# Kernel tuning notes

Hardware: AMD Instinct MI355X
Metric: run time of the kernel (lower is better)

Reference implementation:

```python
import jax, jax.numpy as jnp
import numpy as np

B, L, NW, H, HID, E, NL, DL = 32, 1024, 512, 768, 384, 4, 12, 128


def setup_inputs() -> dict:
    key = jax.random.key(0)
    ks = jax.random.split(key, 16)
    f = lambda k, s: jax.random.normal(k, s, dtype=jnp.float32) * 0.02
    z = lambda s: jnp.zeros(s, jnp.float32)
    return {
        "token_embs": jax.random.normal(ks[0], (B, L, H), dtype=jnp.float32),
        "word_maps": jnp.sort(jax.random.randint(ks[1], (B, L), 0, NW), axis=-1),
        "lang_ids": jax.random.randint(ks[2], (B,), 0, NL),
        # BiLSTM params (PyTorch gate order i,f,g,o packed along dim 0)
        "Wih_f": f(ks[3], (4 * HID, H)), "Whh_f": f(ks[4], (4 * HID, HID)),
        "bih_f": z((4 * HID,)), "bhh_f": z((4 * HID,)),
        "Wih_b": f(ks[5], (4 * HID, H)), "Whh_b": f(ks[6], (4 * HID, HID)),
        "bih_b": z((4 * HID,)), "bhh_b": z((4 * HID,)),
        "proj_W": f(ks[7], (H, 2 * HID)), "proj_b": z((H,)),
        "lang_table": f(ks[8], (NL, DL)),
        "gate_W1": f(ks[9], (H, H + DL)), "gate_b1": z((H,)),
        "gate_W2": f(ks[10], (E, H)), "gate_b2": z((E,)),
        # stacked expert heads: row i is expert i's (H,1) linear
        "ef_W": f(ks[11], (E, H)), "ef_b": z((E,)),
        "ed_W": f(ks[12], (E, H)), "ed_b": z((E,)),
    }


def _seg_mean(embs, wmap):
    # embs: [L, H], wmap: [L] -> [NW, H] per-word mean of subword embeddings
    sums = jax.ops.segment_sum(embs, wmap, num_segments=NW)
    cnt = jax.ops.segment_sum(jnp.ones(embs.shape[:1], embs.dtype), wmap, num_segments=NW)
    return sums / jnp.maximum(cnt, 1.0)[:, None]


def _lstm(x, Wih, Whh, bih, bhh, reverse):
    # x: [B, T, H] -> hidden states [B, T, HID]; gate order i,f,g,o
    def step(carry, xg):
        h, c = carry
        g = xg + h @ Whh.T + bhh
        i, fg, gg, o = jnp.split(g, 4, axis=-1)
        c = jax.nn.sigmoid(fg) * c + jax.nn.sigmoid(i) * jnp.tanh(gg)
        h = jax.nn.sigmoid(o) * jnp.tanh(c)
        return (h, c), h
    xg = jnp.swapaxes(x @ Wih.T + bih, 0, 1)  # [T, B, 4*HID], input proj hoisted
    init = (jnp.zeros((x.shape[0], Whh.shape[1]), x.dtype),) * 2
    _, hs = jax.lax.scan(step, init, xg, reverse=reverse)
    return jnp.swapaxes(hs, 0, 1)


def reference(token_embs, word_maps, lang_ids, Wih_f, Whh_f, bih_f, bhh_f,
              Wih_b, Whh_b, bih_b, bhh_b, proj_W, proj_b, lang_table,
              gate_W1, gate_b1, gate_W2, gate_b2, ef_W, ef_b, ed_W, ed_b):
    # subword -> word segment-mean pooling, batched
    word_embs = jax.vmap(_seg_mean)(token_embs, word_maps)          # [B, NW, H]
    hf = _lstm(word_embs, Wih_f, Whh_f, bih_f, bhh_f, False)        # [B, NW, HID]
    hb = _lstm(word_embs, Wih_b, Whh_b, bih_b, bhh_b, True)         # [B, NW, HID]
    seq = jnp.concatenate([hf, hb], axis=-1) @ proj_W.T + proj_b    # [B, NW, H]
    # dropout omitted (eval mode)
    gate_in = jnp.concatenate([token_embs[:, 0], lang_table[lang_ids]], axis=-1)  # [B, H+DL]
    gate = jax.nn.softmax(
        jax.nn.relu(gate_in @ gate_W1.T + gate_b1) @ gate_W2.T + gate_b2, axis=-1)  # [B, E]
    fix = jnp.einsum('bwe,be->bw', seq @ ef_W.T + ef_b, gate)       # [B, NW]
    dur = jnp.einsum('bwe,be->bw', seq @ ed_W.T + ed_b, gate)       # [B, NW]
    return (fix, dur)
```

## Files before the change

### kernel.cpp

```cpp
#include <hip/hip_runtime.h>
#include <stdint.h>

#define BB 32
#define LL 1024
#define NW 512
#define HH 768
#define HID 384
#define G4 1536
#define EE 4
#define DLL 128
#define GIN 896
#define CWG 12
#define WGC 32
#define HPAD 392

typedef __attribute__((ext_vector_type(8))) short short8;
typedef __attribute__((ext_vector_type(4))) float f32x4;
typedef __attribute__((ext_vector_type(4))) unsigned int u32x4;
typedef __attribute__((ext_vector_type(2))) unsigned int u32x2;

__device__ __forceinline__ float bf2f(short s){
  union { unsigned int u; float f; } v; v.u = ((unsigned int)(unsigned short)s) << 16; return v.f;
}
__device__ __forceinline__ short f2bf(float f){
  union { float f; unsigned int u; } v; v.f = f;
  unsigned int r = v.u + 0x7fffu + ((v.u >> 16) & 1u);
  return (short)(r >> 16);
}
__device__ __forceinline__ float sigm(float x){ return 1.f / (1.f + __expf(-x)); }
__device__ __forceinline__ float ftanh(float x){ float e = __expf(2.f * x); return 1.f - 2.f / (e + 1.f); }

__device__ __forceinline__ void gload16(const void* g, void* l){
  __builtin_amdgcn_global_load_lds(
      (const __attribute__((address_space(1))) unsigned int*)g,
      (__attribute__((address_space(3))) unsigned int*)l, 16, 0, 0);
}

__global__ void k_f2bf(const float* in, short* out, int n){
  int i = blockIdx.x * blockDim.x + threadIdx.x;
  int st = gridDim.x * blockDim.x;
  for (; i < n; i += st) out[i] = f2bf(in[i]);
}

__global__ __launch_bounds__(256) void k_segmean(const float* __restrict__ tok,
                                                 const int* __restrict__ wmap,
                                                 short* __restrict__ we_bf){
  int blk = blockIdx.x;
  int b = blk >> 9;
  int w = blk & 511;
  const int* m = wmap + b * LL;
  int lo = 0, hi = LL;
  while (lo < hi){ int mid = (lo + hi) >> 1; if (m[mid] < w) lo = mid + 1; else hi = mid; }
  int s = lo;
  int lo2 = s, hi2 = LL;
  while (lo2 < hi2){ int mid = (lo2 + hi2) >> 1; if (m[mid] <= w) lo2 = mid + 1; else hi2 = mid; }
  int e = lo2;
  float cnt = (float)(e - s);
  float denom = fmaxf(cnt, 1.f);
  for (int j = threadIdx.x; j < HH; j += 256){
    float acc = 0.f;
    for (int r = s; r < e; ++r) acc += tok[((size_t)b * LL + r) * HH + j];
    we_bf[((size_t)b * NW + w) * HH + j] = f2bf(acc / denom);
  }
}

__global__ __launch_bounds__(256) void k_gemm_bt(const short* __restrict__ Abf,
                                                 const short* __restrict__ Wbf,
                                                 const float* __restrict__ b1,
                                                 const float* __restrict__ b2,
                                                 float* __restrict__ Cf,
                                                 int M, int N, int K){
  __shared__ __attribute__((aligned(16))) short As[128 * 32];
  __shared__ __attribute__((aligned(16))) short Bs[128 * 32];
  int ntiles = N >> 7;
  int m0 = (blockIdx.x / ntiles) << 7;
  int n0 = (blockIdx.x % ntiles) << 7;
  int tid = threadIdx.x, lane = tid & 63, wv = tid >> 6;
  int wm = (wv >> 1) << 6, wn = (wv & 1) << 6;
  f32x4 acc[4][4] = {};
  for (int kk = 0; kk < K; kk += 32){
#pragma unroll
    for (int q = 0; q < 2; ++q){
      int e = q * 256 + tid;
      int row = e >> 2, col = (e & 3) << 3;
      gload16(Abf + (size_t)(m0 + row) * K + kk + col, As + e * 8);
      gload16(Wbf + (size_t)(n0 + row) * K + kk + col, Bs + e * 8);
    }
    __syncthreads();
    short8 af[4], bfr[4];
#pragma unroll
    for (int x = 0; x < 4; ++x){
      af[x]  = *(const short8*)(As + (wm + x * 16 + (lane & 15)) * 32 + ((lane >> 4) << 3));
      bfr[x] = *(const short8*)(Bs + (wn + x * 16 + (lane & 15)) * 32 + ((lane >> 4) << 3));
    }
#pragma unroll
    for (int x = 0; x < 4; ++x)
#pragma unroll
      for (int y = 0; y < 4; ++y)
        acc[x][y] = __builtin_amdgcn_mfma_f32_16x16x32_bf16(af[x], bfr[y], acc[x][y], 0, 0, 0);
    __syncthreads();
  }
#pragma unroll
  for (int x = 0; x < 4; ++x)
#pragma unroll
    for (int y = 0; y < 4; ++y)
#pragma unroll
      for (int i = 0; i < 4; ++i){
        int mm = m0 + wm + x * 16 + ((lane >> 4) << 2) + i;
        int nn = n0 + wn + y * 16 + (lane & 15);
        Cf[(size_t)mm * N + nn] = acc[x][y][i] + b1[nn] + b2[nn];
      }
}

__global__ __launch_bounds__(512) void k_lstm(const float* __restrict__ xg_f,
                                              const float* __restrict__ xg_b,
                                              const short* __restrict__ whh_f,
                                              const short* __restrict__ whh_b,
                                              unsigned int* __restrict__ hbuf,
                                              short* __restrict__ hcat){
  int bx = blockIdx.x;
  int dir = bx / CWG;
  int cg  = bx % CWG;
  int tid = threadIdx.x, lane = tid & 63, wv = tid >> 6;
  int q = lane >> 4, fr = lane & 15;
  int g = wv >> 1, nh = wv & 1;
  int jbase = g * HID + cg * WGC + nh * 16;
  const float* xg  = dir ? xg_b : xg_f;
  const short* whh = dir ? whh_b : whh_f;

  short8 bfrag[12];
  {
    const short* wr = whh + (size_t)(jbase + fr) * HID + q * 8;
#pragma unroll
    for (int ks = 0; ks < 12; ++ks) bfrag[ks] = *(const short8*)(wr + ks * 32);
  }

  __shared__ __attribute__((aligned(16))) short hs[2][16 * HPAD];
  __shared__ float pre[4][16][34];

  float cst0 = 0.f, cst1 = 0.f;
  int eb = tid >> 5, ecol = tid & 31;
  int sc = (tid & 31) * 12;
  unsigned int* hbD = hbuf + (size_t)dir * 2 * 2 * 16 * HID;

  float xgv[4], nxg[4];
  {
    int t0a = dir ? (NW - 1) : 0;
#pragma unroll
    for (int i = 0; i < 4; ++i)
      xgv[i] = xg[((size_t)(q * 4 + i) * NW + t0a) * G4 + jbase + fr];
  }
  u32x4 d0, d1, d2;

  for (int tt = 0; tt < 2 * NW; ++tt){
    int X = tt & 1, t = tt >> 1;
    int t_act = dir ? (NW - 1 - t) : t;
    if (tt > 0){
#pragma unroll
      for (int i = 0; i < 4; ++i) xgv[i] = nxg[i];
    }
    if (t > 0){
      unsigned int pk0 = (d0[0] >> 16) | (d0[1] & 0xffff0000u);
      unsigned int pk1 = (d0[2] >> 16) | (d0[3] & 0xffff0000u);
      unsigned int pk2 = (d1[0] >> 16) | (d1[1] & 0xffff0000u);
      unsigned int pk3 = (d1[2] >> 16) | (d1[3] & 0xffff0000u);
      unsigned int pk4 = (d2[0] >> 16) | (d2[1] & 0xffff0000u);
      unsigned int pk5 = (d2[2] >> 16) | (d2[3] & 0xffff0000u);
      short* dst = &hs[X][eb * HPAD + sc];
      u32x2 w0 = {pk0, pk1}, w1 = {pk2, pk3}, w2 = {pk4, pk5};
      *(u32x2*)(dst)     = w0;
      *(u32x2*)(dst + 4) = w1;
      *(u32x2*)(dst + 8) = w2;
      if (cg == 0){
        int tprev = dir ? (NW - t) : (t - 1);
        short* dh = hcat + ((size_t)(X * 16 + eb) * NW + tprev) * HH + dir * HID + sc;
        *(u32x2*)(dh)     = w0;
        *(u32x2*)(dh + 4) = w1;
        *(u32x2*)(dh + 8) = w2;
      }
    }
    asm volatile("s_waitcnt lgkmcnt(0)" ::: "memory");
    __builtin_amdgcn_s_barrier();
    __builtin_amdgcn_sched_barrier(0);
    f32x4 acc = {}, accB = {};
    if (t > 0){
      const short* hrow = &hs[X][fr * HPAD + q * 8];
#pragma unroll
      for (int ks = 0; ks < 6; ++ks)
        acc  = __builtin_amdgcn_mfma_f32_16x16x32_bf16(*(const short8*)(hrow + ks * 32), bfrag[ks], acc, 0, 0, 0);
#pragma unroll
      for (int ks = 6; ks < 12; ++ks)
        accB = __builtin_amdgcn_mfma_f32_16x16x32_bf16(*(const short8*)(hrow + ks * 32), bfrag[ks], accB, 0, 0, 0);
      acc += accB;
    }
#pragma unroll
    for (int i = 0; i < 4; ++i)
      pre[g][q * 4 + i][nh * 16 + fr] = acc[i] + xgv[i];
    asm volatile("s_waitcnt lgkmcnt(0)" ::: "memory");
    __builtin_amdgcn_s_barrier();
    __builtin_amdgcn_sched_barrier(0);
    float gi2 = pre[0][eb][ecol], gf2 = pre[1][eb][ecol];
    float gg2 = pre[2][eb][ecol], go2 = pre[3][eb][ecol];
    float c = X ? cst1 : cst0;
    c = sigm(gf2) * c + sigm(gi2) * ftanh(gg2);
    float h = sigm(go2) * ftanh(c);
    if (X) cst1 = c; else cst0 = c;
    unsigned int hv = (unsigned int)(unsigned short)f2bf(h);
    unsigned int wtag = (hv << 16) | ((unsigned int)(t + 1) & 0xffffu);
    unsigned int* hw = hbD + ((size_t)X * 2 + (t & 1)) * 16 * HID + eb * HID + cg * WGC + ecol;
    asm volatile("global_store_dword %0, %1, off sc0 sc1" :: "v"(hw), "v"(wtag) : "memory");
    if (t == NW - 1)
      hcat[((size_t)(X * 16 + eb) * NW + t_act) * HH + dir * HID + cg * WGC + ecol] = (short)hv;
    if (tt + 1 < 2 * NW){
      int Xn = (tt + 1) & 1, tn = (tt + 1) >> 1;
      int tna = dir ? (NW - 1 - tn) : tn;
#pragma unroll
      for (int i = 0; i < 4; ++i)
        nxg[i] = xg[((size_t)(Xn * 16 + q * 4 + i) * NW + tna) * G4 + jbase + fr];
      if (tn > 0){
        unsigned int expect = (unsigned int)tn & 0xffffu;
        const unsigned int* hp = hbD + ((size_t)Xn * 2 + ((tn - 1) & 1)) * 16 * HID + eb * HID + sc;
        for (;;){
          asm volatile("global_load_dwordx4 %0, %1, off sc0 sc1" : "=v"(d0) : "v"(hp + 0) : "memory");
          asm volatile("global_load_dwordx4 %0, %1, off sc0 sc1" : "=v"(d1) : "v"(hp + 4) : "memory");
          asm volatile("global_load_dwordx4 %0, %1, off sc0 sc1" : "=v"(d2) : "v"(hp + 8) : "memory");
          asm volatile("s_waitcnt vmcnt(0)" ::: "memory");
          __builtin_amdgcn_sched_barrier(0);
#define TAGBAD(dv) (((dv[0] ^ expect) | (dv[1] ^ expect) | (dv[2] ^ expect) | (dv[3] ^ expect)) & 0xffffu)
          unsigned int bad = TAGBAD(d0) | TAGBAD(d1) | TAGBAD(d2);
#undef TAGBAD
          if (__all(bad == 0)) break;
          __builtin_amdgcn_s_sleep(2);
        }
      }
    }
  }
}

__global__ __launch_bounds__(256) void k_gate(const float* __restrict__ tok,
                                              const int* __restrict__ lids,
                                              const float* __restrict__ ltab,
                                              const float* __restrict__ W1,
                                              const float* __restrict__ b1v,
                                              const float* __restrict__ W2,
                                              const float* __restrict__ b2v,
                                              float* __restrict__ gate){
  __shared__ float gin[GIN];
  __shared__ float hid[HH];
  __shared__ float pr[EE];
  int b = blockIdx.x, tid = threadIdx.x;
  int lid = lids[b];
  for (int i = tid; i < GIN; i += 256)
    gin[i] = (i < HH) ? tok[(size_t)b * LL * HH + i] : ltab[lid * DLL + (i - HH)];
  __syncthreads();
  for (int j = tid; j < HH; j += 256){
    float a = b1v[j];
    const float* wr = W1 + (size_t)j * GIN;
    for (int k = 0; k < GIN; ++k) a += gin[k] * wr[k];
    hid[j] = fmaxf(a, 0.f);
  }
  __syncthreads();
  int wv = tid >> 6, lane = tid & 63;
  if (wv < EE){
    float p = 0.f;
    for (int k = lane; k < HH; k += 64) p += hid[k] * W2[wv * HH + k];
#pragma unroll
    for (int off = 32; off; off >>= 1) p += __shfl_down(p, off);
    if (lane == 0) pr[wv] = p + b2v[wv];
  }
  __syncthreads();
  if (tid == 0){
    float mx = fmaxf(fmaxf(pr[0], pr[1]), fmaxf(pr[2], pr[3]));
    float s = 0.f, ex[EE];
    for (int e2 = 0; e2 < EE; ++e2){ ex[e2] = __expf(pr[e2] - mx); s += ex[e2]; }
    for (int e2 = 0; e2 < EE; ++e2) gate[b * EE + e2] = ex[e2] / s;
  }
}

__global__ __launch_bounds__(256) void k_headpre(const float* __restrict__ efW,
                                                 const float* __restrict__ efb,
                                                 const float* __restrict__ edW,
                                                 const float* __restrict__ edb,
                                                 const float* __restrict__ projW,
                                                 const float* __restrict__ projb,
                                                 float* __restrict__ Acomb,
                                                 float* __restrict__ Ccomb){
  int head = blockIdx.x >> 2, e2 = blockIdx.x & 3, tid = threadIdx.x;
  const float* Wv = head ? edW : efW;
  const float* bv = head ? edb : efb;
  __shared__ float wrow[HH];
  for (int i = tid; i < HH; i += 256) wrow[i] = Wv[e2 * HH + i];
  __syncthreads();
  for (int c = tid; c < HH; c += 256){
    float a = 0.f;
    for (int h2 = 0; h2 < HH; ++h2) a += wrow[h2] * projW[(size_t)h2 * HH + c];
    Acomb[(head * 4 + e2) * HH + c] = a;
  }
  int wv = tid >> 6, lane = tid & 63;
  if (wv == 0){
    float p = 0.f;
    for (int k = lane; k < HH; k += 64) p += wrow[k] * projb[k];
#pragma unroll
    for (int off = 32; off; off >>= 1) p += __shfl_down(p, off);
    if (lane == 0) Ccomb[head * 4 + e2] = p + bv[e2];
  }
}

__global__ __launch_bounds__(256) void k_heads(const short* __restrict__ hcat,
                                               const float* __restrict__ Acomb,
                                               const float* __restrict__ Ccomb,
                                               const float* __restrict__ gate,
                                               float* __restrict__ outp){
  __shared__ float Al[8 * HH];
  int tid = threadIdx.x;
  for (int i = tid; i < 8 * HH; i += 256) Al[i] = Acomb[i];
  __syncthreads();
  int wv = tid >> 6, lane = tid & 63;
  int bw = blockIdx.x * 4 + wv;
  const short* hr = hcat + (size_t)bw * HH;
  float hv[12];
#pragma unroll
  for (int j = 0; j < 12; ++j) hv[j] = bf2f(hr[lane + 64 * j]);
  float dsum[8];
#pragma unroll
  for (int v = 0; v < 8; ++v){
    float p = 0.f;
#pragma unroll
    for (int j = 0; j < 12; ++j) p += hv[j] * Al[v * HH + lane + 64 * j];
#pragma unroll
    for (int off = 32; off; off >>= 1) p += __shfl_xor(p, off);
    dsum[v] = p;
  }
  if (lane == 0){
    int b = bw >> 9;
    float fx = 0.f, du = 0.f;
#pragma unroll
    for (int e2 = 0; e2 < 4; ++e2){
      float g = gate[b * 4 + e2];
      fx += g * (dsum[e2]     + Ccomb[e2]);
      du += g * (dsum[4 + e2] + Ccomb[4 + e2]);
    }
    outp[bw] = fx;
    outp[BB * NW + bw] = du;
  }
}

extern "C" void kernel_launch(void* const* d_in, const int* in_sizes, int n_in,
                              void* d_out, int out_size, void* d_ws, size_t ws_size,
                              hipStream_t stream){
  const float* tok   = (const float*)d_in[0];
  const int*   wmap  = (const int*)d_in[1];
  const int*   lids  = (const int*)d_in[2];
  const float* Wih_f = (const float*)d_in[3];
  const float* Whh_f = (const float*)d_in[4];
  const float* bih_f = (const float*)d_in[5];
  const float* bhh_f = (const float*)d_in[6];
  const float* Wih_b = (const float*)d_in[7];
  const float* Whh_b = (const float*)d_in[8];
  const float* bih_b = (const float*)d_in[9];
  const float* bhh_b = (const float*)d_in[10];
  const float* projW = (const float*)d_in[11];
  const float* projb = (const float*)d_in[12];
  const float* ltab  = (const float*)d_in[13];
  const float* gW1   = (const float*)d_in[14];
  const float* gb1   = (const float*)d_in[15];
  const float* gW2   = (const float*)d_in[16];
  const float* gb2   = (const float*)d_in[17];
  const float* efW   = (const float*)d_in[18];
  const float* efb   = (const float*)d_in[19];
  const float* edW   = (const float*)d_in[20];
  const float* edb   = (const float*)d_in[21];
  float* outp = (float*)d_out;

  char* ws = (char*)d_ws;
  size_t off = 0;
  auto alloc = [&](size_t bytes) -> char* {
    char* p = ws + off;
    off = (off + bytes + 255) & ~(size_t)255;
    return p;
  };
  short* we_bf   = (short*)alloc((size_t)BB * NW * HH * 2);
  short* wihf_bf = (short*)alloc((size_t)G4 * HH * 2);
  short* wihb_bf = (short*)alloc((size_t)G4 * HH * 2);
  short* whhf_bf = (short*)alloc((size_t)G4 * HID * 2);
  short* whhb_bf = (short*)alloc((size_t)G4 * HID * 2);
  float* xg_f    = (float*)alloc((size_t)BB * NW * G4 * 4);
  float* xg_b    = (float*)alloc((size_t)BB * NW * G4 * 4);
  short* hcat    = (short*)alloc((size_t)BB * NW * HH * 2);
  unsigned int* hbuf = (unsigned int*)alloc((size_t)2 * 2 * 2 * 16 * HID * 4);
  float* gateb   = (float*)alloc((size_t)BB * EE * 4);
  float* Acomb   = (float*)alloc((size_t)8 * HH * 4);
  float* Ccomb   = (float*)alloc((size_t)8 * 4);

  k_f2bf<<<1024, 256, 0, stream>>>(Wih_f, wihf_bf, G4 * HH);
  k_f2bf<<<1024, 256, 0, stream>>>(Wih_b, wihb_bf, G4 * HH);
  k_f2bf<<<512, 256, 0, stream>>>(Whh_f, whhf_bf, G4 * HID);
  k_f2bf<<<512, 256, 0, stream>>>(Whh_b, whhb_bf, G4 * HID);
  k_segmean<<<BB * NW, 256, 0, stream>>>(tok, wmap, we_bf);
  k_gemm_bt<<<(BB * NW / 128) * (G4 / 128), 256, 0, stream>>>(we_bf, wihf_bf, bih_f, bhh_f, xg_f, BB * NW, G4, HH);
  k_gemm_bt<<<(BB * NW / 128) * (G4 / 128), 256, 0, stream>>>(we_bf, wihb_bf, bih_b, bhh_b, xg_b, BB * NW, G4, HH);
  k_gate<<<BB, 256, 0, stream>>>(tok, lids, ltab, gW1, gb1, gW2, gb2, gateb);
  k_headpre<<<8, 256, 0, stream>>>(efW, efb, edW, edb, projW, projb, Acomb, Ccomb);
  k_lstm<<<2 * CWG, 512, 0, stream>>>(xg_f, xg_b, whhf_bf, whhb_bf, hbuf, hcat);
  k_heads<<<(BB * NW) / 4, 256, 0, stream>>>(hcat, Acomb, Ccomb, gateb, outp);
}
```

Baseline: 2.580 ms.

## Issue next-step hidden-state and xg loads early, poll after the gate barrier

The speculative loads of the other half-batch's hidden state and input projection now go out right after the MFMA accumulation, before the pre-activation barrier. The tag check and any retry polling move to the top of the next iteration. This is meant to overlap global-memory latency with the barrier and the gate nonlinearity, so the critical path no longer pays for a blocking load right after each store. The first load may catch stale tags more often and need a retry, and the retry sleep is shorter.

```diff
diff --git a/kernel.cpp b/kernel.cpp
--- a/kernel.cpp
+++ b/kernel.cpp
@@ -143,23 +143,36 @@
   int sc = (tid & 31) * 12;
   unsigned int* hbD = hbuf + (size_t)dir * 2 * 2 * 16 * HID;
 
-  float xgv[4], nxg[4];
+  float nxg[4];
   {
     int t0a = dir ? (NW - 1) : 0;
+    const float* xp = xg + (size_t)t0a * G4 + jbase + fr;
 #pragma unroll
     for (int i = 0; i < 4; ++i)
-      xgv[i] = xg[((size_t)(q * 4 + i) * NW + t0a) * G4 + jbase + fr];
+      nxg[i] = xp[(size_t)(q * 4 + i) * NW * G4];
   }
   u32x4 d0, d1, d2;
+  const unsigned int* hp_sav = hbD;
 
   for (int tt = 0; tt < 2 * NW; ++tt){
     int X = tt & 1, t = tt >> 1;
     int t_act = dir ? (NW - 1 - t) : t;
-    if (tt > 0){
-#pragma unroll
-      for (int i = 0; i < 4; ++i) xgv[i] = nxg[i];
-    }
+    asm volatile("s_waitcnt vmcnt(0)" ::: "memory");
+    __builtin_amdgcn_sched_barrier(0);
     if (t > 0){
+      unsigned int expect = (unsigned int)t & 0xffffu;
+      for (;;){
+#define TAGBAD(dv) (((dv[0] ^ expect) | (dv[1] ^ expect) | (dv[2] ^ expect) | (dv[3] ^ expect)) & 0xffffu)
+        unsigned int bad = TAGBAD(d0) | TAGBAD(d1) | TAGBAD(d2);
+#undef TAGBAD
+        if (__all(bad == 0)) break;
+        __builtin_amdgcn_s_sleep(1);
+        asm volatile("global_load_dwordx4 %0, %1, off sc0 sc1" : "=v"(d0) : "v"(hp_sav + 0) : "memory");
+        asm volatile("global_load_dwordx4 %0, %1, off sc0 sc1" : "=v"(d1) : "v"(hp_sav + 4) : "memory");
+        asm volatile("global_load_dwordx4 %0, %1, off sc0 sc1" : "=v"(d2) : "v"(hp_sav + 8) : "memory");
+        asm volatile("s_waitcnt vmcnt(0)" ::: "memory");
+        __builtin_amdgcn_sched_barrier(0);
+      }
       unsigned int pk0 = (d0[0] >> 16) | (d0[1] & 0xffff0000u);
       unsigned int pk1 = (d0[2] >> 16) | (d0[3] & 0xffff0000u);
       unsigned int pk2 = (d1[0] >> 16) | (d1[1] & 0xffff0000u);
@@ -195,7 +208,22 @@
     }
 #pragma unroll
     for (int i = 0; i < 4; ++i)
-      pre[g][q * 4 + i][nh * 16 + fr] = acc[i] + xgv[i];
+      pre[g][q * 4 + i][nh * 16 + fr] = acc[i] + nxg[i];
+    __builtin_amdgcn_sched_barrier(0);
+    if (tt + 1 < 2 * NW){
+      int Xn = 1 - X, tn = X ? (t + 1) : t;
+      int tna = dir ? (NW - 1 - tn) : tn;
+      const float* xp = xg + ((size_t)(Xn * 16) * NW + tna) * G4 + jbase + fr;
+#pragma unroll
+      for (int i = 0; i < 4; ++i)
+        nxg[i] = xp[(size_t)(q * 4 + i) * NW * G4];
+      if (tn > 0){
+        hp_sav = hbD + ((size_t)Xn * 2 + ((tn - 1) & 1)) * 16 * HID + eb * HID + sc;
+        asm volatile("global_load_dwordx4 %0, %1, off sc0 sc1" : "=v"(d0) : "v"(hp_sav + 0) : "memory");
+        asm volatile("global_load_dwordx4 %0, %1, off sc0 sc1" : "=v"(d1) : "v"(hp_sav + 4) : "memory");
+        asm volatile("global_load_dwordx4 %0, %1, off sc0 sc1" : "=v"(d2) : "v"(hp_sav + 8) : "memory");
+      }
+    }
     asm volatile("s_waitcnt lgkmcnt(0)" ::: "memory");
     __builtin_amdgcn_s_barrier();
     __builtin_amdgcn_sched_barrier(0);
@@ -211,29 +239,6 @@
     asm volatile("global_store_dword %0, %1, off sc0 sc1" :: "v"(hw), "v"(wtag) : "memory");
     if (t == NW - 1)
       hcat[((size_t)(X * 16 + eb) * NW + t_act) * HH + dir * HID + cg * WGC + ecol] = (short)hv;
-    if (tt + 1 < 2 * NW){
-      int Xn = (tt + 1) & 1, tn = (tt + 1) >> 1;
-      int tna = dir ? (NW - 1 - tn) : tn;
-#pragma unroll
-      for (int i = 0; i < 4; ++i)
-        nxg[i] = xg[((size_t)(Xn * 16 + q * 4 + i) * NW + tna) * G4 + jbase + fr];
-      if (tn > 0){
-        unsigned int expect = (unsigned int)tn & 0xffffu;
-        const unsigned int* hp = hbD + ((size_t)Xn * 2 + ((tn - 1) & 1)) * 16 * HID + eb * HID + sc;
-        for (;;){
-          asm volatile("global_load_dwordx4 %0, %1, off sc0 sc1" : "=v"(d0) : "v"(hp + 0) : "memory");
-          asm volatile("global_load_dwordx4 %0, %1, off sc0 sc1" : "=v"(d1) : "v"(hp + 4) : "memory");
-          asm volatile("global_load_dwordx4 %0, %1, off sc0 sc1" : "=v"(d2) : "v"(hp + 8) : "memory");
-          asm volatile("s_waitcnt vmcnt(0)" ::: "memory");
-          __builtin_amdgcn_sched_barrier(0);
-#define TAGBAD(dv) (((dv[0] ^ expect) | (dv[1] ^ expect) | (dv[2] ^ expect) | (dv[3] ^ expect)) & 0xffffu)
-          unsigned int bad = TAGBAD(d0) | TAGBAD(d1) | TAGBAD(d2);
-#undef TAGBAD
-          if (__all(bad == 0)) break;
-          __builtin_amdgcn_s_sleep(2);
-        }
-      }
-    }
   }
 }
 
```

Measured after the change: 2.378 ms. 1.08x faster.

## Interleave forward and backward LSTM directions in one workgroup per column group

Applied to the files above, without the earlier changes.

The LSTM kernel now runs both directions in the same workgroup, so 12 workgroups hold both forward and backward recurrent weights in registers and cycle through four independent chains (two directions times two batch halves). Each chain's cross-workgroup h exchange is issued one stage early and waited on with fixed vmcnt counts, so the latency of one chain's global handoff is meant to hide behind the other chains' MFMA and elementwise work. Every workgroup now writes its own h columns straight to hcat each step, replacing the copy done by workgroup 0. In exchange, launch-level parallelism is halved, register pressure roughly doubles, and the hand-counted vmcnt waits are fragile.

```diff
diff --git a/kernel.cpp b/kernel.cpp
--- a/kernel.cpp
+++ b/kernel.cpp
@@ -13,6 +13,7 @@
 #define CWG 12
 #define WGC 32
 #define HPAD 392
+#define HSLOT (16 * HID)
 
 typedef __attribute__((ext_vector_type(8))) short short8;
 typedef __attribute__((ext_vector_type(4))) float f32x4;
@@ -112,128 +113,213 @@
       }
 }
 
+
+#define TB(dv, EXP) (((dv[0] ^ (EXP)) | (dv[1] ^ (EXP)) | (dv[2] ^ (EXP)) | (dv[3] ^ (EXP))) & 0xffffu)
+
+#define HLOAD3(D0, D1, D2, PTR) do{ const unsigned int* _hp = (PTR); \
+  asm volatile("global_load_dwordx4 %0, %1, off sc0 sc1" : "=v"(D0) : "v"(_hp + 0) : "memory"); \
+  asm volatile("global_load_dwordx4 %0, %1, off sc0 sc1" : "=v"(D1) : "v"(_hp + 4) : "memory"); \
+  asm volatile("global_load_dwordx4 %0, %1, off sc0 sc1" : "=v"(D2) : "v"(_hp + 8) : "memory"); }while(0)
+
+#define RETRY3(D0, D1, D2, PTR, EXP) for(;;){ \
+  unsigned int _bad = TB(D0, EXP) | TB(D1, EXP) | TB(D2, EXP); \
+  if (__all(_bad == 0)) break; \
+  __builtin_amdgcn_s_sleep(1); \
+  HLOAD3(D0, D1, D2, PTR); \
+  asm volatile("s_waitcnt vmcnt(0)" ::: "memory"); \
+  __builtin_amdgcn_sched_barrier(0); }
+
+#define STRIP3(D0, D1, D2) do{ \
+  unsigned int _p0 = (D0[0] >> 16) | (D0[1] & 0xffff0000u); \
+  unsigned int _p1 = (D0[2] >> 16) | (D0[3] & 0xffff0000u); \
+  unsigned int _p2 = (D1[0] >> 16) | (D1[1] & 0xffff0000u); \
+  unsigned int _p3 = (D1[2] >> 16) | (D1[3] & 0xffff0000u); \
+  unsigned int _p4 = (D2[0] >> 16) | (D2[1] & 0xffff0000u); \
+  unsigned int _p5 = (D2[2] >> 16) | (D2[3] & 0xffff0000u); \
+  u32x2 _w0 = {_p0, _p1}, _w1 = {_p2, _p3}, _w2 = {_p4, _p5}; \
+  short* _dst = &hs[eb * HPAD + scc]; \
+  *(u32x2*)(_dst)     = _w0; \
+  *(u32x2*)(_dst + 4) = _w1; \
+  *(u32x2*)(_dst + 8) = _w2; }while(0)
+
+#define XG_ISSUE(A0, A1, A2, A3, BASE, XHV, TACT) do{ \
+  const float* _xp = (BASE) + ((size_t)((XHV) * 16 + q * 4) * NW + (TACT)) * G4 + colOff; \
+  asm volatile("global_load_dword %0, %1, off" : "=v"(A0) : "v"(_xp) : "memory"); \
+  asm volatile("global_load_dword %0, %1, off" : "=v"(A1) : "v"(_xp + (size_t)NW * G4) : "memory"); \
+  asm volatile("global_load_dword %0, %1, off" : "=v"(A2) : "v"(_xp + (size_t)2 * NW * G4) : "memory"); \
+  asm volatile("global_load_dword %0, %1, off" : "=v"(A3) : "v"(_xp + (size_t)3 * NW * G4) : "memory"); }while(0)
+
+#define BARRIER_LGKM \
+  asm volatile("s_waitcnt lgkmcnt(0)" ::: "memory"); \
+  __builtin_amdgcn_s_barrier(); \
+  __builtin_amdgcn_sched_barrier(0);
+
+#define MFMA12(BF) { const short* _hr = &hs[fr * HPAD + q * 8]; \
+  _Pragma("unroll") \
+  for (int ks = 0; ks < 6; ++ks) \
+    acc  = __builtin_amdgcn_mfma_f32_16x16x32_bf16(*(const short8*)(_hr + ks * 32), BF[ks], acc, 0, 0, 0); \
+  _Pragma("unroll") \
+  for (int ks = 6; ks < 12; ++ks) \
+    acc2 = __builtin_amdgcn_mfma_f32_16x16x32_bf16(*(const short8*)(_hr + ks * 32), BF[ks], acc2, 0, 0, 0); \
+  acc += acc2; }
+
+#define PREW(A0, A1, A2, A3) \
+  pre[g][q*4+0][nh*16+fr] = acc[0] + (A0); \
+  pre[g][q*4+1][nh*16+fr] = acc[1] + (A1); \
+  pre[g][q*4+2][nh*16+fr] = acc[2] + (A2); \
+  pre[g][q*4+3][nh*16+fr] = acc[3] + (A3);
+
+#define EW_STORE(CST, HBC, TACT, ROWBASE, HCOFF) do{ \
+  float _gi = pre[0][eb][ecol], _gf = pre[1][eb][ecol]; \
+  float _gg = pre[2][eb][ecol], _go = pre[3][eb][ecol]; \
+  CST = sigm(_gf) * CST + sigm(_gi) * ftanh(_gg); \
+  float _h = sigm(_go) * ftanh(CST); \
+  unsigned int _hv = (unsigned int)(unsigned short)f2bf(_h); \
+  unsigned int _wt = (_hv << 16) | ((unsigned int)(j + 1) & 0xffffu); \
+  unsigned int* _hw = (HBC) + (size_t)(j & 1) * HSLOT + stoff; \
+  asm volatile("global_store_dword %0, %1, off sc0 sc1" :: "v"(_hw), "v"(_wt) : "memory"); \
+  short* _hc = hcat + ((size_t)((ROWBASE) + eb) * NW + (TACT)) * HH + (HCOFF); \
+  asm volatile("global_store_short %0, %1, off" :: "v"(_hc), "v"(_hv) : "memory"); }while(0)
+
 __global__ __launch_bounds__(512) void k_lstm(const float* __restrict__ xg_f,
                                               const float* __restrict__ xg_b,
                                               const short* __restrict__ whh_f,
                                               const short* __restrict__ whh_b,
                                               unsigned int* __restrict__ hbuf,
                                               short* __restrict__ hcat){
-  int bx = blockIdx.x;
-  int dir = bx / CWG;
-  int cg  = bx % CWG;
+  int cg = blockIdx.x;
   int tid = threadIdx.x, lane = tid & 63, wv = tid >> 6;
   int q = lane >> 4, fr = lane & 15;
   int g = wv >> 1, nh = wv & 1;
   int jbase = g * HID + cg * WGC + nh * 16;
-  const float* xg  = dir ? xg_b : xg_f;
-  const short* whh = dir ? whh_b : whh_f;
-
-  short8 bfrag[12];
+  int colOff = jbase + fr;
+
+  short8 bfragF[12], bfragB[12];
   {
-    const short* wr = whh + (size_t)(jbase + fr) * HID + q * 8;
-#pragma unroll
-    for (int ks = 0; ks < 12; ++ks) bfrag[ks] = *(const short8*)(wr + ks * 32);
-  }
-
-  __shared__ __attribute__((aligned(16))) short hs[2][16 * HPAD];
+    const short* wrF = whh_f + (size_t)(jbase + fr) * HID + q * 8;
+    const short* wrB = whh_b + (size_t)(jbase + fr) * HID + q * 8;
+#pragma unroll
+    for (int ks = 0; ks < 12; ++ks)
+      asm volatile("global_load_dwordx4 %0, %1, off" : "=v"(bfragF[ks]) : "v"(wrF + ks * 32) : "memory");
+#pragma unroll
+    for (int ks = 0; ks < 12; ++ks)
+      asm volatile("global_load_dwordx4 %0, %1, off" : "=v"(bfragB[ks]) : "v"(wrB + ks * 32) : "memory");
+    asm volatile("s_waitcnt vmcnt(0)" ::: "memory");
+    __builtin_amdgcn_sched_barrier(0);
+  }
+
+  __shared__ __attribute__((aligned(16))) short hs[16 * HPAD];
   __shared__ float pre[4][16][34];
 
-  float cst0 = 0.f, cst1 = 0.f;
   int eb = tid >> 5, ecol = tid & 31;
-  int sc = (tid & 31) * 12;
-  unsigned int* hbD = hbuf + (size_t)dir * 2 * 2 * 16 * HID;
-
-  float xgv[4], nxg[4];
-  {
-    int t0a = dir ? (NW - 1) : 0;
-#pragma unroll
-    for (int i = 0; i < 4; ++i)
-      xgv[i] = xg[((size_t)(q * 4 + i) * NW + t0a) * G4 + jbase + fr];
-  }
-  u32x4 d0, d1, d2;
-
-  for (int tt = 0; tt < 2 * NW; ++tt){
-    int X = tt & 1, t = tt >> 1;
-    int t_act = dir ? (NW - 1 - t) : t;
-    if (tt > 0){
-#pragma unroll
-      for (int i = 0; i < 4; ++i) xgv[i] = nxg[i];
-    }
-    if (t > 0){
-      unsigned int pk0 = (d0[0] >> 16) | (d0[1] & 0xffff0000u);
-      unsigned int pk1 = (d0[2] >> 16) | (d0[3] & 0xffff0000u);
-      unsigned int pk2 = (d1[0] >> 16) | (d1[1] & 0xffff0000u);
-      unsigned int pk3 = (d1[2] >> 16) | (d1[3] & 0xffff0000u);
-      unsigned int pk4 = (d2[0] >> 16) | (d2[1] & 0xffff0000u);
-      unsigned int pk5 = (d2[2] >> 16) | (d2[3] & 0xffff0000u);
-      short* dst = &hs[X][eb * HPAD + sc];
-      u32x2 w0 = {pk0, pk1}, w1 = {pk2, pk3}, w2 = {pk4, pk5};
-      *(u32x2*)(dst)     = w0;
-      *(u32x2*)(dst + 4) = w1;
-      *(u32x2*)(dst + 8) = w2;
-      if (cg == 0){
-        int tprev = dir ? (NW - t) : (t - 1);
-        short* dh = hcat + ((size_t)(X * 16 + eb) * NW + tprev) * HH + dir * HID + sc;
-        *(u32x2*)(dh)     = w0;
-        *(u32x2*)(dh + 4) = w1;
-        *(u32x2*)(dh + 8) = w2;
-      }
-    }
-    asm volatile("s_waitcnt lgkmcnt(0)" ::: "memory");
-    __builtin_amdgcn_s_barrier();
-    __builtin_amdgcn_sched_barrier(0);
-    f32x4 acc = {}, accB = {};
-    if (t > 0){
-      const short* hrow = &hs[X][fr * HPAD + q * 8];
-#pragma unroll
-      for (int ks = 0; ks < 6; ++ks)
-        acc  = __builtin_amdgcn_mfma_f32_16x16x32_bf16(*(const short8*)(hrow + ks * 32), bfrag[ks], acc, 0, 0, 0);
-#pragma unroll
-      for (int ks = 6; ks < 12; ++ks)
-        accB = __builtin_amdgcn_mfma_f32_16x16x32_bf16(*(const short8*)(hrow + ks * 32), bfrag[ks], accB, 0, 0, 0);
-      acc += accB;
-    }
-#pragma unroll
-    for (int i = 0; i < 4; ++i)
-      pre[g][q * 4 + i][nh * 16 + fr] = acc[i] + xgv[i];
-    asm volatile("s_waitcnt lgkmcnt(0)" ::: "memory");
-    __builtin_amdgcn_s_barrier();
-    __builtin_amdgcn_sched_barrier(0);
-    float gi2 = pre[0][eb][ecol], gf2 = pre[1][eb][ecol];
-    float gg2 = pre[2][eb][ecol], go2 = pre[3][eb][ecol];
-    float c = X ? cst1 : cst0;
-    c = sigm(gf2) * c + sigm(gi2) * ftanh(gg2);
-    float h = sigm(go2) * ftanh(c);
-    if (X) cst1 = c; else cst0 = c;
-    unsigned int hv = (unsigned int)(unsigned short)f2bf(h);
-    unsigned int wtag = (hv << 16) | ((unsigned int)(t + 1) & 0xffffu);
-    unsigned int* hw = hbD + ((size_t)X * 2 + (t & 1)) * 16 * HID + eb * HID + cg * WGC + ecol;
-    asm volatile("global_store_dword %0, %1, off sc0 sc1" :: "v"(hw), "v"(wtag) : "memory");
-    if (t == NW - 1)
-      hcat[((size_t)(X * 16 + eb) * NW + t_act) * HH + dir * HID + cg * WGC + ecol] = (short)hv;
-    if (tt + 1 < 2 * NW){
-      int Xn = (tt + 1) & 1, tn = (tt + 1) >> 1;
-      int tna = dir ? (NW - 1 - tn) : tn;
-#pragma unroll
-      for (int i = 0; i < 4; ++i)
-        nxg[i] = xg[((size_t)(Xn * 16 + q * 4 + i) * NW + tna) * G4 + jbase + fr];
-      if (tn > 0){
-        unsigned int expect = (unsigned int)tn & 0xffffu;
-        const unsigned int* hp = hbD + ((size_t)Xn * 2 + ((tn - 1) & 1)) * 16 * HID + eb * HID + sc;
-        for (;;){
-          asm volatile("global_load_dwordx4 %0, %1, off sc0 sc1" : "=v"(d0) : "v"(hp + 0) : "memory");
-          asm volatile("global_load_dwordx4 %0, %1, off sc0 sc1" : "=v"(d1) : "v"(hp + 4) : "memory");
-          asm volatile("global_load_dwordx4 %0, %1, off sc0 sc1" : "=v"(d2) : "v"(hp + 8) : "memory");
-          asm volatile("s_waitcnt vmcnt(0)" ::: "memory");
-          __builtin_amdgcn_sched_barrier(0);
-#define TAGBAD(dv) (((dv[0] ^ expect) | (dv[1] ^ expect) | (dv[2] ^ expect) | (dv[3] ^ expect)) & 0xffffu)
-          unsigned int bad = TAGBAD(d0) | TAGBAD(d1) | TAGBAD(d2);
-#undef TAGBAD
-          if (__all(bad == 0)) break;
-          __builtin_amdgcn_s_sleep(2);
-        }
-      }
-    }
+  int scc = ecol * 12;
+  int ldoff = eb * HID + scc;
+  int stoff = eb * HID + cg * WGC + ecol;
+  int hcOff0 = cg * WGC + ecol;
+  int hcOff1 = HID + cg * WGC + ecol;
+  unsigned int* hb0 = hbuf;
+  unsigned int* hb1 = hbuf + 2 * HSLOT;
+  unsigned int* hb2 = hbuf + 4 * HSLOT;
+  unsigned int* hb3 = hbuf + 6 * HSLOT;
+
+  float c0 = 0.f, c1 = 0.f, c2 = 0.f, c3 = 0.f;
+  float x00, x01, x02, x03, x10, x11, x12, x13;
+  float x20, x21, x22, x23, x30, x31, x32, x33;
+  u32x4 dE0 = {}, dE1 = {}, dE2 = {}, dO0 = {}, dO1 = {}, dO2 = {};
+
+  XG_ISSUE(x00, x01, x02, x03, xg_f, 0, 0);
+  XG_ISSUE(x10, x11, x12, x13, xg_b, 0, NW - 1);
+  XG_ISSUE(x20, x21, x22, x23, xg_f, 1, 0);
+
+  for (int j = 0; j < NW; ++j){
+    int ta0 = j;
+    int ta1 = NW - 1 - j;
+    int ps = (j - 1) & 1;
+    unsigned int expect = (unsigned int)j & 0xffffu;
+
+    if (j == 0)            { asm volatile("s_waitcnt vmcnt(8)"  ::: "memory"); }
+    else if (j == NW - 1)  { asm volatile("s_waitcnt vmcnt(0)"  ::: "memory"); }
+    else                   { asm volatile("s_waitcnt vmcnt(15)" ::: "memory"); }
+    __builtin_amdgcn_sched_barrier(0);
+    if (j > 0){
+      const unsigned int* hpr = hb0 + (size_t)ps * HSLOT + ldoff;
+      RETRY3(dE0, dE1, dE2, hpr, expect);
+      STRIP3(dE0, dE1, dE2);
+    }
+    BARRIER_LGKM;
+    {
+      f32x4 acc = {}, acc2 = {};
+      if (j > 0) MFMA12(bfragF);
+      PREW(x00, x01, x02, x03);
+    }
+    __builtin_amdgcn_sched_barrier(0);
+    if (j >= 1) HLOAD3(dE0, dE1, dE2, hb2 + (size_t)ps * HSLOT + ldoff);
+    XG_ISSUE(x30, x31, x32, x33, xg_b, 1, ta1);
+    BARRIER_LGKM;
+    EW_STORE(c0, hb0, ta0, 0, hcOff0);
+
+    if (j == 0)            { asm volatile("s_waitcnt vmcnt(10)" ::: "memory"); }
+    else if (j == NW - 1)  { asm volatile("s_waitcnt vmcnt(0)"  ::: "memory"); }
+    else                   { asm volatile("s_waitcnt vmcnt(15)" ::: "memory"); }
+    __builtin_amdgcn_sched_barrier(0);
+    if (j > 0){
+      const unsigned int* hpr = hb1 + (size_t)ps * HSLOT + ldoff;
+      RETRY3(dO0, dO1, dO2, hpr, expect);
+      STRIP3(dO0, dO1, dO2);
+    }
+    BARRIER_LGKM;
+    {
+      f32x4 acc = {}, acc2 = {};
+      if (j > 0) MFMA12(bfragB);
+      PREW(x10, x11, x12, x13);
+    }
+    __builtin_amdgcn_sched_barrier(0);
+    if (j >= 1) HLOAD3(dO0, dO1, dO2, hb3 + (size_t)ps * HSLOT + ldoff);
+    if (j + 1 < NW) XG_ISSUE(x00, x01, x02, x03, xg_f, 0, j + 1);
+    BARRIER_LGKM;
+    EW_STORE(c1, hb1, ta1, 0, hcOff1);
+
+    if (j == 0)            { asm volatile("s_waitcnt vmcnt(12)" ::: "memory"); }
+    else if (j == NW - 1)  { asm volatile("s_waitcnt vmcnt(0)"  ::: "memory"); }
+    else                   { asm volatile("s_waitcnt vmcnt(15)" ::: "memory"); }
+    __builtin_amdgcn_sched_barrier(0);
+    if (j > 0){
+      const unsigned int* hpr = hb2 + (size_t)ps * HSLOT + ldoff;
+      RETRY3(dE0, dE1, dE2, hpr, expect);
+      STRIP3(dE0, dE1, dE2);
+    }
+    BARRIER_LGKM;
+    {
+      f32x4 acc = {}, acc2 = {};
+      if (j > 0) MFMA12(bfragF);
+      PREW(x20, x21, x22, x23);
+    }
+    __builtin_amdgcn_sched_barrier(0);
+    if (j + 1 < NW) HLOAD3(dE0, dE1, dE2, hb0 + (size_t)(j & 1) * HSLOT + ldoff);
+    if (j + 1 < NW) XG_ISSUE(x10, x11, x12, x13, xg_b, 0, NW - 2 - j);
+    BARRIER_LGKM;
+    EW_STORE(c2, hb2, ta0, 16, hcOff0);
+
+    if (j == 0)            { asm volatile("s_waitcnt vmcnt(17)" ::: "memory"); }
+    else if (j == NW - 1)  { asm volatile("s_waitcnt vmcnt(0)"  ::: "memory"); }
+    else                   { asm volatile("s_waitcnt vmcnt(15)" ::: "memory"); }
+    __builtin_amdgcn_sched_barrier(0);
+    if (j > 0){
+      const unsigned int* hpr = hb3 + (size_t)ps * HSLOT + ldoff;
+      RETRY3(dO0, dO1, dO2, hpr, expect);
+      STRIP3(dO0, dO1, dO2);
+    }
+    BARRIER_LGKM;
+    {
+      f32x4 acc = {}, acc2 = {};
+      if (j > 0) MFMA12(bfragB);
+      PREW(x30, x31, x32, x33);
+    }
+    __builtin_amdgcn_sched_barrier(0);
+    if (j + 1 < NW) HLOAD3(dO0, dO1, dO2, hb1 + (size_t)(j & 1) * HSLOT + ldoff);
+    if (j + 1 < NW) XG_ISSUE(x20, x21, x22, x23, xg_f, 1, j + 1);
+    BARRIER_LGKM;
+    EW_STORE(c3, hb3, ta1, 16, hcOff1);
   }
 }
 
@@ -387,7 +473,7 @@
   float* xg_f    = (float*)alloc((size_t)BB * NW * G4 * 4);
   float* xg_b    = (float*)alloc((size_t)BB * NW * G4 * 4);
   short* hcat    = (short*)alloc((size_t)BB * NW * HH * 2);
-  unsigned int* hbuf = (unsigned int*)alloc((size_t)2 * 2 * 2 * 16 * HID * 4);
+  unsigned int* hbuf = (unsigned int*)alloc((size_t)4 * 2 * HSLOT * 4);
   float* gateb   = (float*)alloc((size_t)BB * EE * 4);
   float* Acomb   = (float*)alloc((size_t)8 * HH * 4);
   float* Ccomb   = (float*)alloc((size_t)8 * 4);
@@ -401,6 +487,6 @@
   k_gemm_bt<<<(BB * NW / 128) * (G4 / 128), 256, 0, stream>>>(we_bf, wihb_bf, bih_b, bhh_b, xg_b, BB * NW, G4, HH);
   k_gate<<<BB, 256, 0, stream>>>(tok, lids, ltab, gW1, gb1, gW2, gb2, gateb);
   k_headpre<<<8, 256, 0, stream>>>(efW, efb, edW, edb, projW, projb, Acomb, Ccomb);
-  k_lstm<<<2 * CWG, 512, 0, stream>>>(xg_f, xg_b, whhf_bf, whhb_bf, hbuf, hcat);
+  k_lstm<<<CWG, 512, 0, stream>>>(xg_f, xg_b, whhf_bf, whhb_bf, hbuf, hcat);
   k_heads<<<(BB * NW) / 4, 256, 0, stream>>>(hcat, Acomb, Ccomb, gateb, outp);
 }
```

New measurement: 3.671 ms, median of 3. 42.3% more time.
